# Kernel tuning notes

Measured on AMD Instinct MI355X. Metric: run time of the kernel, lower is better.

## Reference

```python
import jax, jax.numpy as jnp
import numpy as np

N, E, F_IN, D, K = 100000, 1600000, 4, 64, 5

def gelu(x):
    return jax.nn.gelu(x, approximate=False)  # torch F.gelu default (erf)

def mlp(x, w1, b1, w2, b2):
    return gelu(x @ w1 + b1) @ w2 + b2

def cheb_conv(x, w, b, src, tgt, norm, n):
    # PyG ChebConv with sym normalization, lambda_max=2.0 (default):
    # scaled Laplacian L_hat = L - I has zero diagonal, off-diag = -w_norm.
    def prop(h):
        return jax.ops.segment_sum(norm[:, None] * h[src], tgt, num_segments=n)
    Tx0 = x
    out = Tx0 @ w[0]
    Tx1 = prop(Tx0)
    out = out + Tx1 @ w[1]
    for k in range(2, w.shape[0]):
        Tx2 = 2.0 * prop(Tx1) - Tx0
        out = out + Tx2 @ w[k]
        Tx0, Tx1 = Tx1, Tx2
    return out + b

def cheb_residual(x, cw1, cb1, cw2, cb2, lw, lb, src, tgt, norm, n):
    t = gelu(cheb_conv(x, cw1, cb1, src, tgt, norm, n))
    f = cheb_conv(t, cw2, cb2, src, tgt, norm, n)
    return gelu(f + x @ lw + lb)


def setup_inputs() -> dict:
    key = jax.random.key(0)
    ks = jax.random.split(key, 18)
    p = lambda k, shape: jax.random.normal(k, shape, dtype=jnp.float32) * 0.05
    return {
        "x": jax.random.normal(ks[0], (N, F_IN), dtype=jnp.float32),
        "edge_index": jax.random.randint(ks[1], (2, E), 0, N, dtype=jnp.int32),
        "edge_attr": jax.random.uniform(ks[2], (E,), dtype=jnp.float32),
        "e1_w": p(ks[3], (F_IN, D)), "e1_b": p(ks[4], (D,)),
        "e2_w": p(ks[5], (D, D)), "e2_b": p(ks[6], (D,)),
        "cw1": p(ks[7], (3, K, D, D)), "cb1": p(ks[8], (3, D)),
        "cw2": p(ks[9], (3, K, D, D)), "cb2": p(ks[10], (3, D)),
        "lw": p(ks[11], (3, D, D)), "lb": p(ks[12], (3, D)),
        "d1_w": p(ks[13], (D, 1)), "d1_b": p(ks[14], (1,)),
        "d2_w": p(ks[15], (1, 1)), "d2_b": p(ks[16], (1,)),
    }


def reference(x, edge_index, edge_attr, e1_w, e1_b, e2_w, e2_b,
              cw1, cb1, cw2, cb2, lw, lb, d1_w, d1_b, d2_w, d2_b):
    n = x.shape[0]
    src, tgt = edge_index[0], edge_index[1]
    # sym-normalized Laplacian edge weights (get_laplacian 'sym')
    deg = jax.ops.segment_sum(edge_attr, src, num_segments=n)
    dis = jnp.where(deg > 0, jax.lax.rsqrt(jnp.where(deg > 0, deg, 1.0)), 0.0)
    norm = -edge_attr * dis[src] * dis[tgt]  # scaled by 2/lambda_max = 1
    h = gelu(mlp(x, e1_w, e1_b, e2_w, e2_b))  # node_embed + gelu
    for b in range(3):  # c3, c4, c5 (c6 unused in original forward)
        h = cheb_residual(h, cw1[b], cb1[b], cw2[b], cb2[b], lw[b], lb[b], src, tgt, norm, n)
    return mlp(h, d1_w, d1_b, d2_w, d2_b)  # node_down -> [N, 1]
```

## Files before the change

kernel.cpp:

```cpp
#include <hip/hip_runtime.h>
#include <hip/hip_fp16.h>
#include <math.h>


#define PSTR 48

typedef _Float16 f16x8 __attribute__((ext_vector_type(8)));
typedef float f32x4 __attribute__((ext_vector_type(4)));

__device__ __forceinline__ float gelu_f(float v) {
  return 0.5f * v * (1.0f + erff(v * 0.70710678118654752440f));
}

__global__ __launch_bounds__(256) void k_deg(const int* __restrict__ src,
                                             const float* __restrict__ ea,
                                             float* __restrict__ deg, int E) {
  int e = blockIdx.x * 256 + threadIdx.x;
  if (e < E) atomicAdd(&deg[src[e]], ea[e]);
}

__global__ __launch_bounds__(256) void k_dis(float* __restrict__ deg, int n) {
  int i = blockIdx.x * 256 + threadIdx.x;
  if (i < n) {
    float d = deg[i];
    deg[i] = (d > 0.f) ? rsqrtf(d) : 0.f;
  }
}

__global__ __launch_bounds__(256) void k_fill(
    const int* __restrict__ src, const int* __restrict__ tgt,
    const float* __restrict__ ea, const float* __restrict__ dis,
    int* __restrict__ cur, unsigned long long* __restrict__ pair, int E) {
  int e = blockIdx.x * 256 + threadIdx.x;
  if (e < E) {
    int s = src[e], t = tgt[e];
    int pos = atomicAdd(&cur[t], 1);
    if (pos < PSTR) {
      float w = -ea[e] * dis[s] * dis[t];
      unsigned long long v =
          (unsigned long long)(unsigned int)s |
          ((unsigned long long)__float_as_uint(w) << 32);
      pair[(size_t)t * PSTR + pos] = v;
    }
  }
}

__global__ __launch_bounds__(256) void k_encode(
    const float* __restrict__ x, const float* __restrict__ w1,
    const float* __restrict__ b1, const float* __restrict__ w2,
    const float* __restrict__ b2, __half* __restrict__ h16, int n) {
  __shared__ float sw1[4 * 64];
  __shared__ float sb1[64];
  __shared__ float sw2[64 * 64];
  __shared__ float sb2[64];
  __shared__ float smid[4][64];
  if (threadIdx.x < 256) sw1[threadIdx.x] = w1[threadIdx.x];
  if (threadIdx.x < 64) {
    sb1[threadIdx.x] = b1[threadIdx.x];
    sb2[threadIdx.x] = b2[threadIdx.x];
  }
  for (int i = threadIdx.x; i < 4096; i += 256) sw2[i] = w2[i];
  __syncthreads();
  const int wave = threadIdx.x >> 6;
  const int lane = threadIdx.x & 63;
  for (int base = blockIdx.x * 4; base < n; base += gridDim.x * 4) {
    const int node = base + wave;
    const bool ok = node < n;
    float m = 0.f;
    if (ok) {
      const float4 xv = *(const float4*)(x + (size_t)node * 4);
      m = xv.x * sw1[lane] + xv.y * sw1[64 + lane] + xv.z * sw1[128 + lane] +
          xv.w * sw1[192 + lane] + sb1[lane];
      m = gelu_f(m);
    }
    smid[wave][lane] = m;
    __syncthreads();
    float o = sb2[lane];
#pragma unroll 8
    for (int k = 0; k < 64; ++k) o += smid[wave][k] * sw2[k * 64 + lane];
    if (ok) h16[(size_t)node * 64 + lane] = __float2half_rn(gelu_f(o));
    __syncthreads();
  }
}

template <bool HASPREV>
__global__ __launch_bounds__(256) void k_prop(
    const __half* __restrict__ hin16, const int* __restrict__ cnt,
    const unsigned long long* __restrict__ pair,
    const __half* __restrict__ prev16, __half* __restrict__ out16, int n) {
  const int wid = (int)((blockIdx.x * 256 + threadIdx.x) >> 6);
  const int lane = threadIdx.x & 63;
  const int hl = lane & 31;
  const int node = (wid << 1) + (lane >> 5);
  if ((wid << 1) >= n) return;
  const bool ok = node < n;
  const int deg = ok ? min(cnt[node], PSTR) : 0;
  const size_t pbase = (size_t)node * PSTR;
  const int sbase = lane & 32;
  float accx = 0.f, accy = 0.f;
  for (int j0 = 0; __any(j0 < deg); j0 += 16) {
    int idx = 0;
    float w = 0.f;
    const int slot = j0 + (hl & 15);
    if (slot < deg) {
      const unsigned long long v =
          __builtin_nontemporal_load(pair + pbase + slot);
      idx = (int)(unsigned int)v;
      w = __uint_as_float((unsigned int)(v >> 32));
    }
#pragma unroll
    for (int u = 0; u < 16; ++u) {
      const int bidx = __shfl(idx, sbase + u, 64);
      const float bw = __shfl(w, sbase + u, 64);
      const __half2 hv =
          *(const __half2*)(hin16 + ((size_t)bidx << 6) + (hl << 1));
      const float2 f = __half22float2(hv);
      accx = fmaf(bw, f.x, accx);
      accy = fmaf(bw, f.y, accy);
    }
  }
  if (ok) {
    float rx = accx, ry = accy;
    if (HASPREV) {
      const float2 pf = __half22float2(
          *(const __half2*)(prev16 + ((size_t)node << 6) + (hl << 1)));
      rx = 2.f * accx - pf.x;
      ry = 2.f * accy - pf.y;
    }
    *(__half2*)(out16 + ((size_t)node << 6) + (hl << 1)) =
        __floats2half2_rn(rx, ry);
  }
}

template <int TOT, bool HASEX, bool GELU>
__global__ __launch_bounds__(512) void k_gemm_mfma(
    const __half* __restrict__ A0, const __half* __restrict__ Atx,
    const float* __restrict__ Wb, const __half* __restrict__ Aex,
    const float* __restrict__ Wex, const float* __restrict__ bias1,
    const float* __restrict__ bias2, __half* __restrict__ out16, int n) {
  __shared__ __align__(16) _Float16 sWh[TOT * 2 * 4 * 64 * 8];
  const int tid = threadIdx.x;
  for (int b = 0; b < TOT; ++b) {
    const float* Wp = (b < 5) ? Wb + b * 4096 : Wex;
    for (int idx = tid; idx < 4096; idx += 512) {
      const int k = idx >> 6, nn = idx & 63;
      const int lane = (nn & 15) | (((k >> 3) & 3) << 4);
      const int dst =
          (((b * 2 + (k >> 5)) * 4 + (nn >> 4)) * 64 + lane) * 8 + (k & 7);
      sWh[dst] = (_Float16)Wp[idx];
    }
  }
  __syncthreads();

  const int wv = tid >> 6;
  const int lane = tid & 63;
  const int kg = lane >> 4;
  const int row = blockIdx.x * 128 + wv * 16 + (lane & 15);
  const bool rok = row < n;
  const size_t n64 = (size_t)n * 64;
  const f16x8* bw = (const f16x8*)sWh;

  f32x4 acc[4];
#pragma unroll
  for (int ct = 0; ct < 4; ++ct) acc[ct] = (f32x4){0.f, 0.f, 0.f, 0.f};

  for (int b = 0; b < TOT; ++b) {
    const __half* Ap =
        (b == 0) ? A0 : (b < 5 ? Atx + (size_t)(b - 1) * n64 : Aex);
    f16x8 a0 = {}, a1 = {};
    if (rok) {
      a0 = *(const f16x8*)(Ap + (size_t)row * 64 + kg * 8);
      a1 = *(const f16x8*)(Ap + (size_t)row * 64 + 32 + kg * 8);
    }
#pragma unroll
    for (int ct = 0; ct < 4; ++ct) {
      const f16x8 b0 = bw[((b * 2 + 0) * 4 + ct) * 64 + lane];
      const f16x8 b1 = bw[((b * 2 + 1) * 4 + ct) * 64 + lane];
      acc[ct] = __builtin_amdgcn_mfma_f32_16x16x32_f16(a0, b0, acc[ct], 0, 0, 0);
      acc[ct] = __builtin_amdgcn_mfma_f32_16x16x32_f16(a1, b1, acc[ct], 0, 0, 0);
    }
  }

  const int orow0 = blockIdx.x * 128 + wv * 16 + (lane >> 4) * 4;
#pragma unroll
  for (int ct = 0; ct < 4; ++ct) {
    const int col = ct * 16 + (lane & 15);
    float bb = bias1[col];
    if (HASEX) bb += bias2[col];
#pragma unroll
    for (int j = 0; j < 4; ++j) {
      const int r = orow0 + j;
      if (r < n) {
        float v = acc[ct][j] + bb;
        if (GELU) v = gelu_f(v);
        out16[(size_t)r * 64 + col] = __float2half_rn(v);
      }
    }
  }
}

__global__ __launch_bounds__(256) void k_decode(
    const __half* __restrict__ h16, const float* __restrict__ d1w,
    const float* __restrict__ d1b, const float* __restrict__ d2w,
    const float* __restrict__ d2b, float* __restrict__ out, int n) {
  const int q = (blockIdx.x * 256 + threadIdx.x) >> 4;
  const int l = threadIdx.x & 15;
  if (q >= n) return;
  union { short4 s; __half2 h[2]; } u;
  u.s = *(const short4*)(h16 + (size_t)q * 64 + l * 4);
  const float2 v01 = __half22float2(u.h[0]);
  const float2 v23 = __half22float2(u.h[1]);
  const float4 w = *(const float4*)(d1w + l * 4);
  float s = v01.x * w.x + v01.y * w.y + v23.x * w.z + v23.y * w.w;
  s += __shfl_xor(s, 1, 64);
  s += __shfl_xor(s, 2, 64);
  s += __shfl_xor(s, 4, 64);
  s += __shfl_xor(s, 8, 64);
  if (l == 0) out[q] = gelu_f(s + d1b[0]) * d2w[0] + d2b[0];
}

extern "C" void kernel_launch(void* const* d_in, const int* in_sizes, int n_in,
                              void* d_out, int out_size, void* d_ws,
                              size_t ws_size, hipStream_t stream) {
  const float* x = (const float*)d_in[0];
  const int* ei = (const int*)d_in[1];
  const float* ea = (const float*)d_in[2];
  const float* e1w = (const float*)d_in[3];
  const float* e1b = (const float*)d_in[4];
  const float* e2w = (const float*)d_in[5];
  const float* e2b = (const float*)d_in[6];
  const float* cw1 = (const float*)d_in[7];
  const float* cb1 = (const float*)d_in[8];
  const float* cw2 = (const float*)d_in[9];
  const float* cb2 = (const float*)d_in[10];
  const float* lw = (const float*)d_in[11];
  const float* lb = (const float*)d_in[12];
  const float* d1w = (const float*)d_in[13];
  const float* d1b = (const float*)d_in[14];
  const float* d2w = (const float*)d_in[15];
  const float* d2b = (const float*)d_in[16];

  const int N = in_sizes[0] / 4;
  const int E = in_sizes[2];
  const int* src = ei;
  const int* tgt = ei + E;

  char* p = (char*)d_ws;
  auto carve = [&](size_t bytes) -> char* {
    char* r = p;
    p += (bytes + 255) & ~(size_t)255;
    return r;
  };
  float* deg = (float*)carve((size_t)N * 4);
  int* cur = (int*)carve((size_t)N * 4);
  unsigned long long* pair =
      (unsigned long long*)carve((size_t)N * PSTR * 8);
  __half* h16 = (__half*)carve((size_t)N * 64 * 2);
  __half* t16 = (__half*)carve((size_t)N * 64 * 2);
  __half* Tx16 = (__half*)carve((size_t)4 * N * 64 * 2);
  (void)ws_size;

  hipMemsetAsync(deg, 0, (size_t)N * 4, stream);
  hipMemsetAsync(cur, 0, (size_t)N * 4, stream);

  const int gE = (E + 255) / 256;
  const int gN = (N + 255) / 256;
  k_deg<<<gE, 256, 0, stream>>>(src, ea, deg, E);
  k_dis<<<gN, 256, 0, stream>>>(deg, N);
  k_fill<<<gE, 256, 0, stream>>>(src, tgt, ea, deg, cur, pair, E);
  k_encode<<<2048, 256, 0, stream>>>(x, e1w, e1b, e2w, e2b, h16, N);

  const size_t n64 = (size_t)N * 64;
  const int gP = (N + 7) / 8;
  const int gG = (N + 127) / 128;
  __half* Tx1 = Tx16;
  __half* Tx2 = Tx16 + n64;
  __half* Tx3 = Tx16 + 2 * n64;
  __half* Tx4 = Tx16 + 3 * n64;
  for (int b = 0; b < 3; ++b) {
    const float* cw1b = cw1 + (size_t)b * 5 * 4096;
    const float* cb1b = cb1 + b * 64;
    const float* cw2b = cw2 + (size_t)b * 5 * 4096;
    const float* cb2b = cb2 + b * 64;
    const float* lwb = lw + (size_t)b * 4096;
    const float* lbb = lb + b * 64;

    k_prop<false><<<gP, 256, 0, stream>>>(h16, cur, pair, nullptr, Tx1, N);
    k_prop<true><<<gP, 256, 0, stream>>>(Tx1, cur, pair, h16, Tx2, N);
    k_prop<true><<<gP, 256, 0, stream>>>(Tx2, cur, pair, Tx1, Tx3, N);
    k_prop<true><<<gP, 256, 0, stream>>>(Tx3, cur, pair, Tx2, Tx4, N);
    k_gemm_mfma<5, false, true><<<gG, 512, 0, stream>>>(
        h16, Tx16, cw1b, nullptr, nullptr, cb1b, nullptr, t16, N);

    k_prop<false><<<gP, 256, 0, stream>>>(t16, cur, pair, nullptr, Tx1, N);
    k_prop<true><<<gP, 256, 0, stream>>>(Tx1, cur, pair, t16, Tx2, N);
    k_prop<true><<<gP, 256, 0, stream>>>(Tx2, cur, pair, Tx1, Tx3, N);
    k_prop<true><<<gP, 256, 0, stream>>>(Tx3, cur, pair, Tx2, Tx4, N);
    k_gemm_mfma<6, true, true><<<gG, 512, 0, stream>>>(
        t16, Tx16, cw2b, h16, lwb, cb2b, lbb, h16, N);
  }

  const int gD = (int)(((size_t)N * 16 + 255) / 256);
  k_decode<<<gD, 256, 0, stream>>>(h16, d1w, d1b, d2w, d2b, (float*)d_out, N);
}
```

Measured before the change: 1.203 ms.

## Process four nodes per wave in propagation with 8-byte feature gathers

The propagation kernel now assigns 16 lanes per node, so four nodes share a wave instead of two. Each lane loads 4 halfs (8 bytes) per neighbour instead of 2, and the launch grid halves. The loop runs full 16-edge chunks up to the wave-max degree, then a partial remainder loop, instead of always padding to 16. This aims to cut per-edge shuffle and instruction overhead and wasted padded iterations, at the cost of more registers and more imbalance across nodes within a wave.

```diff
diff --git a/kernel.cpp b/kernel.cpp
--- a/kernel.cpp
+++ b/kernel.cpp
@@ -90,18 +90,23 @@
     const __half* __restrict__ prev16, __half* __restrict__ out16, int n) {
   const int wid = (int)((blockIdx.x * 256 + threadIdx.x) >> 6);
   const int lane = threadIdx.x & 63;
-  const int hl = lane & 31;
-  const int node = (wid << 1) + (lane >> 5);
-  if ((wid << 1) >= n) return;
+  const int ql = lane & 15;
+  const int qb = lane & 48;
+  const int node = (wid << 2) + (lane >> 4);
+  if ((wid << 2) >= n) return;
   const bool ok = node < n;
   const int deg = ok ? min(cnt[node], PSTR) : 0;
   const size_t pbase = (size_t)node * PSTR;
-  const int sbase = lane & 32;
-  float accx = 0.f, accy = 0.f;
-  for (int j0 = 0; __any(j0 < deg); j0 += 16) {
+  int dmax = deg;
+  dmax = max(dmax, __shfl_xor(dmax, 16, 64));
+  dmax = max(dmax, __shfl_xor(dmax, 32, 64));
+
+  float acc0 = 0.f, acc1 = 0.f, acc2 = 0.f, acc3 = 0.f;
+  int j0 = 0;
+  for (; j0 + 16 <= dmax; j0 += 16) {
+    const int slot = j0 + ql;
     int idx = 0;
     float w = 0.f;
-    const int slot = j0 + (hl & 15);
     if (slot < deg) {
       const unsigned long long v =
           __builtin_nontemporal_load(pair + pbase + slot);
@@ -110,25 +115,62 @@
     }
 #pragma unroll
     for (int u = 0; u < 16; ++u) {
-      const int bidx = __shfl(idx, sbase + u, 64);
-      const float bw = __shfl(w, sbase + u, 64);
-      const __half2 hv =
-          *(const __half2*)(hin16 + ((size_t)bidx << 6) + (hl << 1));
-      const float2 f = __half22float2(hv);
-      accx = fmaf(bw, f.x, accx);
-      accy = fmaf(bw, f.y, accy);
-    }
-  }
+      const int bidx = __shfl(idx, qb | u, 64);
+      const float bw = __shfl(w, qb | u, 64);
+      union { unsigned long long q; __half2 h[2]; } hv;
+      hv.q = *(const unsigned long long*)(hin16 + ((size_t)bidx << 6) +
+                                          (ql << 2));
+      const float2 f01 = __half22float2(hv.h[0]);
+      const float2 f23 = __half22float2(hv.h[1]);
+      acc0 = fmaf(bw, f01.x, acc0);
+      acc1 = fmaf(bw, f01.y, acc1);
+      acc2 = fmaf(bw, f23.x, acc2);
+      acc3 = fmaf(bw, f23.y, acc3);
+    }
+  }
+  if (j0 < dmax) {
+    const int slot = j0 + ql;
+    int idx = 0;
+    float w = 0.f;
+    if (slot < deg) {
+      const unsigned long long v =
+          __builtin_nontemporal_load(pair + pbase + slot);
+      idx = (int)(unsigned int)v;
+      w = __uint_as_float((unsigned int)(v >> 32));
+    }
+    const int rem = dmax - j0;
+#pragma unroll 4
+    for (int u = 0; u < rem; ++u) {
+      const int bidx = __shfl(idx, qb | u, 64);
+      const float bw = __shfl(w, qb | u, 64);
+      union { unsigned long long q; __half2 h[2]; } hv;
+      hv.q = *(const unsigned long long*)(hin16 + ((size_t)bidx << 6) +
+                                          (ql << 2));
+      const float2 f01 = __half22float2(hv.h[0]);
+      const float2 f23 = __half22float2(hv.h[1]);
+      acc0 = fmaf(bw, f01.x, acc0);
+      acc1 = fmaf(bw, f01.y, acc1);
+      acc2 = fmaf(bw, f23.x, acc2);
+      acc3 = fmaf(bw, f23.y, acc3);
+    }
+  }
+
   if (ok) {
-    float rx = accx, ry = accy;
     if (HASPREV) {
-      const float2 pf = __half22float2(
-          *(const __half2*)(prev16 + ((size_t)node << 6) + (hl << 1)));
-      rx = 2.f * accx - pf.x;
-      ry = 2.f * accy - pf.y;
-    }
-    *(__half2*)(out16 + ((size_t)node << 6) + (hl << 1)) =
-        __floats2half2_rn(rx, ry);
+      union { unsigned long long q; __half2 h[2]; } pv;
+      pv.q = *(const unsigned long long*)(prev16 + ((size_t)node << 6) +
+                                          (ql << 2));
+      const float2 p01 = __half22float2(pv.h[0]);
+      const float2 p23 = __half22float2(pv.h[1]);
+      acc0 = 2.f * acc0 - p01.x;
+      acc1 = 2.f * acc1 - p01.y;
+      acc2 = 2.f * acc2 - p23.x;
+      acc3 = 2.f * acc3 - p23.y;
+    }
+    union { unsigned long long q; __half2 h[2]; } ov;
+    ov.h[0] = __floats2half2_rn(acc0, acc1);
+    ov.h[1] = __floats2half2_rn(acc2, acc3);
+    *(unsigned long long*)(out16 + ((size_t)node << 6) + (ql << 2)) = ov.q;
   }
 }
 
@@ -271,7 +313,7 @@
   k_encode<<<2048, 256, 0, stream>>>(x, e1w, e1b, e2w, e2b, h16, N);
 
   const size_t n64 = (size_t)N * 64;
-  const int gP = (N + 7) / 8;
+  const int gP = (N + 15) / 16;
   const int gG = (N + 127) / 128;
   __half* Tx1 = Tx16;
   __half* Tx2 = Tx16 + n64;
```

Measured after the change: 1.221 ms. About the same (+1.5%).

## Use one wave per node with scalar pair loads in Chebyshev propagation

Applied to the files above, without the earlier changes.

The propagation kernel now maps one 64-lane wave to each node, one lane per feature, instead of two nodes per wave with half2 lanes and shuffle-broadcast edge lists. Edge (index, weight) pairs are read eight at a time as wave-uniform loads with no bounds check. The pair buffer is zeroed up front so that padded slots contribute zero weight. This removes the shuffles and per-slot branching, but it doubles the number of waves, uses 16-bit per-lane gathers instead of 32-bit ones, and adds a large memset of the pair table.

```diff
diff --git a/kernel.cpp b/kernel.cpp
--- a/kernel.cpp
+++ b/kernel.cpp
@@ -88,48 +88,36 @@
     const __half* __restrict__ hin16, const int* __restrict__ cnt,
     const unsigned long long* __restrict__ pair,
     const __half* __restrict__ prev16, __half* __restrict__ out16, int n) {
-  const int wid = (int)((blockIdx.x * 256 + threadIdx.x) >> 6);
+  const int node = (int)((blockIdx.x * 256 + threadIdx.x) >> 6);
   const int lane = threadIdx.x & 63;
-  const int hl = lane & 31;
-  const int node = (wid << 1) + (lane >> 5);
-  if ((wid << 1) >= n) return;
-  const bool ok = node < n;
-  const int deg = ok ? min(cnt[node], PSTR) : 0;
-  const size_t pbase = (size_t)node * PSTR;
-  const int sbase = lane & 32;
-  float accx = 0.f, accy = 0.f;
-  for (int j0 = 0; __any(j0 < deg); j0 += 16) {
-    int idx = 0;
-    float w = 0.f;
-    const int slot = j0 + (hl & 15);
-    if (slot < deg) {
-      const unsigned long long v =
-          __builtin_nontemporal_load(pair + pbase + slot);
-      idx = (int)(unsigned int)v;
-      w = __uint_as_float((unsigned int)(v >> 32));
-    }
-#pragma unroll
-    for (int u = 0; u < 16; ++u) {
-      const int bidx = __shfl(idx, sbase + u, 64);
-      const float bw = __shfl(w, sbase + u, 64);
-      const __half2 hv =
-          *(const __half2*)(hin16 + ((size_t)bidx << 6) + (hl << 1));
-      const float2 f = __half22float2(hv);
-      accx = fmaf(bw, f.x, accx);
-      accy = fmaf(bw, f.y, accy);
-    }
-  }
-  if (ok) {
-    float rx = accx, ry = accy;
-    if (HASPREV) {
-      const float2 pf = __half22float2(
-          *(const __half2*)(prev16 + ((size_t)node << 6) + (hl << 1)));
-      rx = 2.f * accx - pf.x;
-      ry = 2.f * accy - pf.y;
-    }
-    *(__half2*)(out16 + ((size_t)node << 6) + (hl << 1)) =
-        __floats2half2_rn(rx, ry);
-  }
+  if (node >= n) return;
+  const int deg = min(cnt[node], PSTR);
+  const unsigned long long* __restrict__ prow = pair + (size_t)node * PSTR;
+  float acc = 0.f;
+  for (int j = 0; j < deg; j += 8) {
+    unsigned long long p0 = prow[j + 0];
+    unsigned long long p1 = prow[j + 1];
+    unsigned long long p2 = prow[j + 2];
+    unsigned long long p3 = prow[j + 3];
+    unsigned long long p4 = prow[j + 4];
+    unsigned long long p5 = prow[j + 5];
+    unsigned long long p6 = prow[j + 6];
+    unsigned long long p7 = prow[j + 7];
+#define EDGE(P)                                                       \
+  {                                                                   \
+    const int idx_ = (int)(unsigned int)(P);                          \
+    const float w_ = __uint_as_float((unsigned int)((P) >> 32));      \
+    acc = fmaf(w_, __half2float(hin16[((size_t)idx_ << 6) + lane]),   \
+               acc);                                                  \
+  }
+    EDGE(p0) EDGE(p1) EDGE(p2) EDGE(p3)
+    EDGE(p4) EDGE(p5) EDGE(p6) EDGE(p7)
+#undef EDGE
+  }
+  float r = acc;
+  if (HASPREV)
+    r = 2.f * acc - __half2float(prev16[((size_t)node << 6) + lane]);
+  out16[((size_t)node << 6) + lane] = __float2half_rn(r);
 }
 
 template <int TOT, bool HASEX, bool GELU>
@@ -262,6 +250,7 @@
 
   hipMemsetAsync(deg, 0, (size_t)N * 4, stream);
   hipMemsetAsync(cur, 0, (size_t)N * 4, stream);
+  hipMemsetAsync(pair, 0, (size_t)N * PSTR * 8, stream);
 
   const int gE = (E + 255) / 256;
   const int gN = (N + 255) / 256;
@@ -271,7 +260,7 @@
   k_encode<<<2048, 256, 0, stream>>>(x, e1w, e1b, e2w, e2b, h16, N);
 
   const size_t n64 = (size_t)N * 64;
-  const int gP = (N + 7) / 8;
+  const int gP = (N + 3) / 4;
   const int gG = (N + 127) / 128;
   __half* Tx1 = Tx16;
   __half* Tx2 = Tx16 + n64;
```

Measured after the change: 1.552 ms. 1.29x slower.

## Assign one node per wave in prop, splitting edges across half-waves

Applied to the files above, without the earlier changes.

The propagation kernel now maps one node per 64-lane wave instead of two. The two half-waves each take alternating edges, and the partial sums are combined with a cross-half shuffle. Edge pairs are read with wave-uniform scalar loads rather than per-lane loads plus 16 shuffles, and the degree is made uniform through readfirstlane. The pair buffer is zeroed up front so that padded odd slots contribute zero. The cost is twice as many waves, an extra large memset each call, and possibly uninitialized padding if the odd slot lies beyond PSTR.

```diff
diff --git a/kernel.cpp b/kernel.cpp
--- a/kernel.cpp
+++ b/kernel.cpp
@@ -88,44 +88,42 @@
     const __half* __restrict__ hin16, const int* __restrict__ cnt,
     const unsigned long long* __restrict__ pair,
     const __half* __restrict__ prev16, __half* __restrict__ out16, int n) {
-  const int wid = (int)((blockIdx.x * 256 + threadIdx.x) >> 6);
+  int node = (int)(blockIdx.x * 4 + (threadIdx.x >> 6));
+  node = __builtin_amdgcn_readfirstlane(node);
+  if (node >= n) return;
   const int lane = threadIdx.x & 63;
   const int hl = lane & 31;
-  const int node = (wid << 1) + (lane >> 5);
-  if ((wid << 1) >= n) return;
-  const bool ok = node < n;
-  const int deg = ok ? min(cnt[node], PSTR) : 0;
-  const size_t pbase = (size_t)node * PSTR;
-  const int sbase = lane & 32;
-  float accx = 0.f, accy = 0.f;
-  for (int j0 = 0; __any(j0 < deg); j0 += 16) {
-    int idx = 0;
-    float w = 0.f;
-    const int slot = j0 + (hl & 15);
-    if (slot < deg) {
-      const unsigned long long v =
-          __builtin_nontemporal_load(pair + pbase + slot);
-      idx = (int)(unsigned int)v;
-      w = __uint_as_float((unsigned int)(v >> 32));
-    }
-#pragma unroll
-    for (int u = 0; u < 16; ++u) {
-      const int bidx = __shfl(idx, sbase + u, 64);
-      const float bw = __shfl(w, sbase + u, 64);
-      const __half2 hv =
-          *(const __half2*)(hin16 + ((size_t)bidx << 6) + (hl << 1));
-      const float2 f = __half22float2(hv);
-      accx = fmaf(bw, f.x, accx);
-      accy = fmaf(bw, f.y, accy);
-    }
-  }
-  if (ok) {
-    float rx = accx, ry = accy;
+  const int sel = lane >> 5;
+  const int deg = __builtin_amdgcn_readfirstlane(min(cnt[node], PSTR));
+  const unsigned long long* __restrict__ prow = pair + (size_t)node * PSTR;
+
+  float ax = 0.f, ay = 0.f;
+  const int dceil = (deg + 1) & ~1;
+#pragma unroll 4
+  for (int j = 0; j < dceil; j += 2) {
+    const unsigned long long p0 = prow[j];
+    const unsigned long long p1 = prow[j + 1];
+    const int i0 = (int)(unsigned int)p0;
+    const int i1 = (int)(unsigned int)p1;
+    const float w0 = __uint_as_float((unsigned int)(p0 >> 32));
+    const float w1 = __uint_as_float((unsigned int)(p1 >> 32));
+    const int bidx = sel ? i1 : i0;
+    const float bw = sel ? w1 : w0;
+    const __half2 hv =
+        *(const __half2*)(hin16 + ((size_t)bidx << 6) + (hl << 1));
+    const float2 f = __half22float2(hv);
+    ax = fmaf(bw, f.x, ax);
+    ay = fmaf(bw, f.y, ay);
+  }
+  ax += __shfl_xor(ax, 32, 64);
+  ay += __shfl_xor(ay, 32, 64);
+  if (lane < 32) {
+    float rx = ax, ry = ay;
     if (HASPREV) {
       const float2 pf = __half22float2(
           *(const __half2*)(prev16 + ((size_t)node << 6) + (hl << 1)));
-      rx = 2.f * accx - pf.x;
-      ry = 2.f * accy - pf.y;
+      rx = 2.f * ax - pf.x;
+      ry = 2.f * ay - pf.y;
     }
     *(__half2*)(out16 + ((size_t)node << 6) + (hl << 1)) =
         __floats2half2_rn(rx, ry);
@@ -262,6 +260,7 @@
 
   hipMemsetAsync(deg, 0, (size_t)N * 4, stream);
   hipMemsetAsync(cur, 0, (size_t)N * 4, stream);
+  hipMemsetAsync(pair, 0, (size_t)N * PSTR * 8, stream);
 
   const int gE = (E + 255) / 256;
   const int gN = (N + 255) / 256;
@@ -271,7 +270,7 @@
   k_encode<<<2048, 256, 0, stream>>>(x, e1w, e1b, e2w, e2b, h16, N);
 
   const size_t n64 = (size_t)N * 64;
-  const int gP = (N + 7) / 8;
+  const int gP = (N + 3) / 4;
   const int gG = (N + 127) / 128;
   __half* Tx1 = Tx16;
   __half* Tx2 = Tx16 + n64;
```

After: 1.423 ms. 18.3% more time.
